# Optimization experiments

Measured on AMD Instinct MI355X. Metric: run time of the kernel, lower is better.

## Reference

```python
import jax, jax.numpy as jnp
import numpy as np

NUM_HEADS = 16
D_MODEL = 1024
D_K = D_MODEL // NUM_HEADS
MAX_SEQ_LEN = 4096
ROPE_BASE = 10000.0
BATCH = 2
SEQ_LEN = 2048


def _rope_tables(seq_len, d_k, base=ROPE_BASE):
    # theta_i = 1 / base^(2i/d_k), i = 0..d_k/2-1
    theta = 1.0 / base ** (jnp.arange(0, d_k, 2, dtype=jnp.float32) / d_k)
    m = jnp.arange(seq_len, dtype=jnp.float32)
    m_theta = jnp.outer(m, theta)                      # [S, d_k/2]
    ang = jnp.concatenate([m_theta, m_theta], axis=-1)  # [S, d_k]
    return jnp.cos(ang), jnp.sin(ang)


def _apply_rope(x, cos, sin):
    # x: [B, H, S, d_k]; rotate-half: cat(-x2, x1)
    d2 = x.shape[-1] // 2
    x1, x2 = x[..., :d2], x[..., d2:]
    x_flip = jnp.concatenate([-x2, x1], axis=-1)
    return x * cos + x_flip * sin


def setup_inputs() -> dict:
    key = jax.random.key(0)
    kx, kq, kk, kv, ko = jax.random.split(key, 5)
    s = 1.0 / np.sqrt(D_MODEL)  # ~ nn.Linear default init scale
    x = jax.random.normal(kx, (BATCH, SEQ_LEN, D_MODEL), dtype=jnp.float32)
    W_Q = jax.random.uniform(kq, (D_MODEL, D_MODEL), jnp.float32, -s, s)
    W_K = jax.random.uniform(kk, (D_MODEL, D_MODEL), jnp.float32, -s, s)
    W_V = jax.random.uniform(kv, (D_MODEL, D_MODEL), jnp.float32, -s, s)
    W_O = jax.random.uniform(ko, (D_MODEL, D_MODEL), jnp.float32, -s, s)
    return {"x": x, "W_Q": W_Q, "W_K": W_K, "W_V": W_V, "W_O": W_O}


def reference(x, W_Q, W_K, W_V, W_O):
    B, S, _ = x.shape
    # Linear with weight [out, in]: y = x @ W.T
    def proj(W):
        y = jnp.einsum('bsd,ed->bse', x, W)
        return y.reshape(B, S, NUM_HEADS, D_K).transpose(0, 2, 1, 3)  # [B,H,S,dk]
    Q, K, V = proj(W_Q), proj(W_K), proj(W_V)
    cos, sin = _rope_tables(S, D_K)
    Q = _apply_rope(Q, cos, sin)
    K = _apply_rope(K, cos, sin)
    scores = jnp.einsum('bhsd,bhtd->bhst', Q, K) / jnp.sqrt(jnp.float32(D_K))
    causal = jnp.tril(jnp.ones((S, S), dtype=bool))
    scores = jnp.where(causal[None, None], scores, -jnp.inf)
    attn = jax.nn.softmax(scores, axis=-1)
    out = jnp.einsum('bhst,bhtd->bhsd', attn, V)
    out = out.transpose(0, 2, 1, 3).reshape(B, S, D_MODEL)
    return jnp.einsum('bsd,ed->bse', out, W_O)
```

## Files before the change

### kernel.cpp

```cpp
#include <hip/hip_runtime.h>
#include <hip/hip_bf16.h>

#define BATCH 2
#define SEQ 2048
#define DM 1024
#define NH 16
#define DKH 64

typedef __attribute__((ext_vector_type(8))) __bf16 bf16x8;
typedef __attribute__((ext_vector_type(4))) float f32x4;
typedef __attribute__((ext_vector_type(2))) float f32x2;
typedef __attribute__((ext_vector_type(8))) unsigned short ushort8;

__device__ __forceinline__ void gload16(const void* g, void* l) {
  __builtin_amdgcn_global_load_lds(
      (const __attribute__((address_space(1))) void*)g,
      (__attribute__((address_space(3))) void*)l, 16, 0, 0);
}

__global__ void prep(const float* __restrict__ x,
                     const float* __restrict__ w0, const float* __restrict__ w1,
                     const float* __restrict__ w2, const float* __restrict__ w3,
                     __bf16* __restrict__ xb, __bf16* __restrict__ wb,
                     float* __restrict__ tab) {
  const int bid = blockIdx.x, tid = threadIdx.x;
  if (bid < 2048) {
    int i = bid * 256 + tid;
    f32x4 a = ((const f32x4*)x)[2 * i], b = ((const f32x4*)x)[2 * i + 1];
    bf16x8 o;
    o[0]=(__bf16)a[0]; o[1]=(__bf16)a[1]; o[2]=(__bf16)a[2]; o[3]=(__bf16)a[3];
    o[4]=(__bf16)b[0]; o[5]=(__bf16)b[1]; o[6]=(__bf16)b[2]; o[7]=(__bf16)b[3];
    ((bf16x8*)xb)[i] = o;
  } else if (bid < 4096) {
    int i = (bid - 2048) * 256 + tid;
    int wi = i >> 17;
    const float* src = (wi == 0) ? w0 : (wi == 1) ? w1 : (wi == 2) ? w2 : w3;
    int li = i & 131071;
    f32x4 a = ((const f32x4*)src)[2 * li], b = ((const f32x4*)src)[2 * li + 1];
    bf16x8 o;
    o[0]=(__bf16)a[0]; o[1]=(__bf16)a[1]; o[2]=(__bf16)a[2]; o[3]=(__bf16)a[3];
    o[4]=(__bf16)b[0]; o[5]=(__bf16)b[1]; o[6]=(__bf16)b[2]; o[7]=(__bf16)b[3];
    ((bf16x8*)wb)[i] = o;
  } else {
    int idx = (bid - 4096) * 256 + tid;
    int s = idx >> 5, ii = idx & 31;
    float theta = exp2f((float)ii * -0.41524101186092029f);
    float sn, c;
    sincosf((float)s * theta, &sn, &c);
    tab[2 * idx] = c;
    tab[2 * idx + 1] = sn;
  }
}

#define QSCALE 0.1803368801111137f

template<int EPI, int BN>
__launch_bounds__(256, 3)
__global__ void gemm_bt(const __bf16* __restrict__ A, const __bf16* __restrict__ B,
                        void* __restrict__ Cout, int M, int N, int K,
                        const float* __restrict__ tab) {
  __shared__ __bf16 As[128 * 64];
  __shared__ __bf16 Bs[BN * 64];
  const int tid = threadIdx.x;
  const int lane = tid & 63;
  const int w = tid >> 6;
  const int wr = w >> 1, wc = w & 1;
  const int fr = lane & 15, fq = lane >> 4;
  const int lid = blockIdx.y * gridDim.x + blockIdx.x;
  const int total = gridDim.x * gridDim.y;
  const int nlid = (lid >> 3) + (lid & 7) * (total >> 3);
  const int bx = nlid & 31;
  const int by = nlid >> 5;
  const int m0 = bx * 128;
  const int n0 = by * BN;
  const int NFR = BN / 32;

  f32x4 acc[4][BN / 32] = {};
  const int NT = K >> 6;

  for (int kt = 0; kt < NT; ++kt) {
    const int k0 = kt << 6;
    __syncthreads();
    #pragma unroll
    for (int p = 0; p < 4; ++p) {
      int c = p * 256 + tid;
      int row = c >> 3, cs = (c & 7) ^ (row & 7);
      gload16(&A[(size_t)(m0 + row) * K + k0 + cs * 8], &As[(p * 256 + w * 64) * 8]);
    }
    #pragma unroll
    for (int p = 0; p < BN / 32; ++p) {
      int c = p * 256 + tid;
      int row = c >> 3, cs = (c & 7) ^ (row & 7);
      gload16(&B[(size_t)(n0 + row) * K + k0 + cs * 8], &Bs[(p * 256 + w * 64) * 8]);
    }
    __syncthreads();
    #pragma unroll
    for (int kk = 0; kk < 2; ++kk) {
      bf16x8 af[4], bfr[BN / 32];
      #pragma unroll
      for (int mf = 0; mf < 4; ++mf) {
        int row = wr * 64 + mf * 16 + fr;
        af[mf] = *(const bf16x8*)&As[row * 64 + ((kk * 32 + fq * 8) ^ ((fr & 7) << 3))];
      }
      #pragma unroll
      for (int nf = 0; nf < NFR; ++nf) {
        int row = wc * (BN / 2) + nf * 16 + fr;
        bfr[nf] = *(const bf16x8*)&Bs[row * 64 + ((kk * 32 + fq * 8) ^ ((fr & 7) << 3))];
      }
      __builtin_amdgcn_s_setprio(1);
      #pragma unroll
      for (int mf = 0; mf < 4; ++mf)
        #pragma unroll
        for (int nf = 0; nf < NFR; ++nf)
          acc[mf][nf] = __builtin_amdgcn_mfma_f32_16x16x32_bf16(af[mf], bfr[nf], acc[mf][nf], 0, 0, 0);
      __builtin_amdgcn_s_setprio(0);
    }
  }

  if (EPI == 0) {
    const int nbase = n0 + wc * 64;
    const int which = nbase >> 10;
    const int h = (nbase & 1023) >> 6;
    const int b = m0 >> 11;
    __bf16* base0 = (__bf16*)Cout + (size_t)which * (4u << 20);
    if (which < 2) {
      const float scale = (which == 0) ? QSCALE : 1.0f;
      __bf16* dst = base0 + ((size_t)(b * NH + h)) * SEQ * DKH;
      #pragma unroll
      for (int mf = 0; mf < 4; ++mf) {
        #pragma unroll
        for (int j = 0; j < 4; ++j) {
          int s = (m0 & (SEQ - 1)) + wr * 64 + mf * 16 + fq * 4 + j;
          #pragma unroll
          for (int nf = 0; nf < 2; ++nf) {
            int i = nf * 16 + fr;
            f32x2 cs = ((const f32x2*)tab)[s * 32 + i];
            float a = acc[mf][nf][j], bb = acc[mf][nf + 2][j];
            dst[(size_t)s * DKH + i]      = (__bf16)((a * cs[0] - bb * cs[1]) * scale);
            dst[(size_t)s * DKH + i + 32] = (__bf16)((bb * cs[0] + a * cs[1]) * scale);
          }
        }
      }
    } else {
      __bf16* dst = base0 + ((size_t)(b * NH + h)) * DKH * SEQ;
      #pragma unroll
      for (int mf = 0; mf < 4; ++mf) {
        #pragma unroll
        for (int nf = 0; nf < 4; ++nf) {
          int dk = nf * 16 + fr;
          #pragma unroll
          for (int j = 0; j < 4; ++j) {
            int sp = (m0 & (SEQ - 1)) + wr * 64 + (mf >> 1) * 32 + fq * 8 + (mf & 1) * 4 + j;
            dst[(size_t)dk * SEQ + sp] = (__bf16)acc[mf][nf][j];
          }
        }
      }
    }
  } else {
    #pragma unroll
    for (int mf = 0; mf < 4; ++mf)
      #pragma unroll
      for (int nf = 0; nf < NFR; ++nf)
        #pragma unroll
        for (int j = 0; j < 4; ++j) {
          int m = m0 + wr * 64 + mf * 16 + fq * 4 + j;
          int n = n0 + wc * (BN / 2) + nf * 16 + fr;
          ((float*)Cout)[(size_t)m * N + n] = acc[mf][nf][j];
        }
  }
}

__launch_bounds__(512, 4)
__global__ void attn_causal(const __bf16* __restrict__ Qg, const __bf16* __restrict__ Kg,
                            const __bf16* __restrict__ Vtg, __bf16* __restrict__ Out,
                            float* __restrict__ P0, float* __restrict__ P1,
                            float* __restrict__ L0, float* __restrict__ L1) {
  __shared__ __bf16 Ks[2][128 * 64];
  __shared__ __bf16 Vts[2][64 * 128];
  const int tid = threadIdx.x;
  const int lane = tid & 63;
  const int w = tid >> 6;
  const int fr = lane & 15, fq = lane >> 4;
  const int r = blockIdx.x;
  const int nlid = (r & 7) * 64 + (r >> 3);
  const int bh = nlid >> 4;
  const int slot = nlid & 15;
  const bool isA = slot < 8;
  const int qa = slot;
  const int qb = isA ? (15 - slot) : slot;
  const int sw  = isA ? (qa + 1) : 99;
  const int off = isA ? (8 - qa) : 0;
  const int nst = isA ? 8 : 9;
  const int b = bh >> 4, h = bh & 15;
  const __bf16* Qh = Qg + (size_t)bh * SEQ * DKH;
  const __bf16* Kh = Kg + (size_t)bh * SEQ * DKH;
  const __bf16* Vth = Vtg + (size_t)bh * DKH * SEQ;

  int qrow_lo = (isA ? qa : qb) * 128 + w * 16;

  const int ck0 = tid, ck1 = 512 + tid;
  const int kr0 = ck0 >> 3, kc0 = ((ck0 & 7) ^ (kr0 & 7)) * 8;
  const int kr1 = ck1 >> 3, kc1 = ((ck1 & 7) ^ (kr1 & 7)) * 8;
  const int vd0 = ck0 >> 4, vk0 = (((ck0 & 15) & 8) | (((ck0 & 15) ^ vd0) & 7)) * 8;
  const int vd1 = ck1 >> 4, vk1 = (((ck1 & 15) & 8) | (((ck1 & 15) ^ vd1) & 7)) * 8;

#define STAGE(buf, kvt) {                                                     \
    const int ts_ = (kvt) << 7;                                               \
    gload16(&Kh[(size_t)(ts_ + kr0) * DKH + kc0], &Ks[buf][(w * 64) * 8]);    \
    gload16(&Kh[(size_t)(ts_ + kr1) * DKH + kc1], &Ks[buf][(512 + w * 64) * 8]); \
    gload16(&Vth[(size_t)vd0 * SEQ + ts_ + vk0], &Vts[buf][(w * 64) * 8]);    \
    gload16(&Vth[(size_t)vd1 * SEQ + ts_ + vk1], &Vts[buf][(512 + w * 64) * 8]); }

  bf16x8 qf[2];
  #pragma unroll
  for (int kk = 0; kk < 2; ++kk)
    qf[kk] = *(const bf16x8*)&Qh[(size_t)(qrow_lo + fr) * DKH + kk * 32 + fq * 8];

  f32x4 Oa[4] = {};
  float lsum = 0.f;

  STAGE(0, 0);
  __syncthreads();

  for (int it = 0; it < 9; ++it) {
    const int cur = it & 1;
    if (it + 1 < nst) {
      const int nx = it + 1;
      const int kvn = (nx < sw) ? nx : nx + off;
      STAGE(cur ^ 1, kvn);
    }
    if (isA && it == sw) {
      float ls = lsum;
      ls += __shfl_xor(ls, 16);
      ls += __shfl_xor(ls, 32);
      float rl[4];
      #pragma unroll
      for (int j = 0; j < 4; ++j)
        rl[j] = 1.0f / __shfl(ls, fq * 4 + j);
      #pragma unroll
      for (int nf = 0; nf < 4; ++nf)
        #pragma unroll
        for (int j = 0; j < 4; ++j) {
          int qr = qrow_lo + fq * 4 + j;
          Out[((size_t)(b * SEQ) + qr) * DM + h * DKH + nf * 16 + fr] =
              (__bf16)(Oa[nf][j] * rl[j]);
        }
      #pragma unroll
      for (int nf = 0; nf < 4; ++nf) Oa[nf] = (f32x4){0.f, 0.f, 0.f, 0.f};
      lsum = 0.f;
      qrow_lo = qb * 128 + w * 16;
      #pragma unroll
      for (int kk = 0; kk < 2; ++kk)
        qf[kk] = *(const bf16x8*)&Qh[(size_t)(qrow_lo + fr) * DKH + kk * 32 + fq * 8];
    }
    if (it < nst) {
      const int kvt = (it < sw) ? it : it + off;
      #pragma unroll
      for (int sub = 0; sub < 2; ++sub) {
        const int ts = (kvt << 7) + (sub << 6);
        if (ts > qrow_lo + 15) continue;
        f32x4 sacc[4] = {};
        __builtin_amdgcn_s_setprio(1);
        #pragma unroll
        for (int kk = 0; kk < 2; ++kk) {
          #pragma unroll
          for (int nf = 0; nf < 4; ++nf) {
            int krow = (sub << 6) + nf * 16 + fr;
            bf16x8 kf = *(const bf16x8*)&Ks[cur][krow * 64 + ((kk * 32 + fq * 8) ^ ((fr & 7) << 3))];
            sacc[nf] = __builtin_amdgcn_mfma_f32_16x16x32_bf16(kf, qf[kk], sacc[nf], 0, 0, 0);
          }
        }
        __builtin_amdgcn_s_setprio(0);
        const bool need_mask = (ts + 63 > qrow_lo);
        if (need_mask) {
          const int qr = qrow_lo + fr;
          #pragma unroll
          for (int nf = 0; nf < 4; ++nf) {
            #pragma unroll
            for (int j = 0; j < 4; ++j) {
              float v = sacc[nf][j];
              int tc = ts + nf * 16 + fq * 4 + j;
              if (tc > qr) v = -INFINITY;
              float pv = exp2f(v);
              lsum += pv;
              sacc[nf][j] = pv;
            }
          }
        } else {
          #pragma unroll
          for (int nf = 0; nf < 4; ++nf) {
            #pragma unroll
            for (int j = 0; j < 4; ++j) {
              float pv = exp2f(sacc[nf][j]);
              lsum += pv;
              sacc[nf][j] = pv;
            }
          }
        }
        bf16x8 pa[2];
        #pragma unroll
        for (int kk = 0; kk < 2; ++kk)
          #pragma unroll
          for (int e = 0; e < 8; ++e)
            pa[kk][e] = (__bf16)sacc[2 * kk + (e >> 2)][e & 3];
        __builtin_amdgcn_s_setprio(1);
        #pragma unroll
        for (int kk = 0; kk < 2; ++kk) {
          #pragma unroll
          for (int nf = 0; nf < 4; ++nf) {
            int d = nf * 16 + fr;
            bf16x8 vf = *(const bf16x8*)&Vts[cur][d * 128 + (sub << 6) +
                         (((kk * 4 + fq) ^ (fr & 7)) << 3)];
            Oa[nf] = __builtin_amdgcn_mfma_f32_16x16x32_bf16(pa[kk], vf, Oa[nf], 0, 0, 0);
          }
        }
        __builtin_amdgcn_s_setprio(0);
      }
    }
    __syncthreads();
  }
#undef STAGE
  float* P = isA ? P1 : P0;
  float* L = isA ? L1 : L0;
  const int rbase = ((bh << 3) + (qb - 8)) << 7;
  float ls = lsum;
  ls += __shfl_xor(ls, 16);
  ls += __shfl_xor(ls, 32);
  if (lane < 16) L[rbase + w * 16 + lane] = ls;
  #pragma unroll
  for (int nf = 0; nf < 4; ++nf)
    #pragma unroll
    for (int j = 0; j < 4; ++j)
      P[(size_t)(rbase + w * 16 + fq * 4 + j) * 64 + nf * 16 + fr] = Oa[nf][j];
}

__global__ void combine(const float* __restrict__ P0, const float* __restrict__ P1,
                        const float* __restrict__ L0, const float* __restrict__ L1,
                        __bf16* __restrict__ Ab) {
  int t = blockIdx.x * blockDim.x + threadIdx.x;
  int rowid = t >> 3, d0 = (t & 7) * 8;
  int bh = rowid >> 10, rem = rowid & 1023;
  int tq = rem >> 7, r = rem & 127;
  float rl = 1.0f / (L0[rowid] + L1[rowid]);
  const float* p0 = P0 + (size_t)rowid * 64 + d0;
  const float* p1 = P1 + (size_t)rowid * 64 + d0;
  f32x4 a0 = *(const f32x4*)p0, a1 = *(const f32x4*)(p0 + 4);
  f32x4 b0 = *(const f32x4*)p1, b1 = *(const f32x4*)(p1 + 4);
  bf16x8 o;
  #pragma unroll
  for (int e = 0; e < 4; ++e) {
    o[e]     = (__bf16)((a0[e] + b0[e]) * rl);
    o[e + 4] = (__bf16)((a1[e] + b1[e]) * rl);
  }
  int s = (tq + 8) * 128 + r;
  int b = bh >> 4, h = bh & 15;
  *(bf16x8*)&Ab[((size_t)b * SEQ + s) * DM + h * DKH + d0] = o;
}

extern "C" void kernel_launch(void* const* d_in, const int* in_sizes, int n_in,
                              void* d_out, int out_size, void* d_ws, size_t ws_size,
                              hipStream_t stream) {
  const float* x  = (const float*)d_in[0];
  const float* Wq = (const float*)d_in[1];
  const float* Wk = (const float*)d_in[2];
  const float* Wv = (const float*)d_in[3];
  const float* Wo = (const float*)d_in[4];

  char* ws = (char*)d_ws;
  __bf16* xb  = (__bf16*)(ws);
  __bf16* wqb = (__bf16*)(ws + ( 8u << 20));
  __bf16* wob = (__bf16*)(ws + (14u << 20));
  __bf16* Qb  = (__bf16*)(ws + (16u << 20));
  __bf16* Kb  = (__bf16*)(ws + (24u << 20));
  __bf16* Vtb = (__bf16*)(ws + (32u << 20));
  __bf16* Ab  = (__bf16*)(ws + (40u << 20));
  float*  tab = (float*)(ws + (48u << 20));
  float*  L0  = (float*)(ws + (49u << 20));
  float*  L1  = (float*)(ws + (49u << 20) + (1u << 18));
  float* P0 = (float*)d_out;
  float* P1 = P0 + (32768 * 64);

  prep<<<dim3(4352), dim3(256), 0, stream>>>(x, Wq, Wk, Wv, Wo, xb, wqb, tab);

  gemm_bt<0, 128><<<dim3(32, 24), dim3(256), 0, stream>>>(xb, wqb, Qb, BATCH * SEQ, 3 * DM, DM, tab);

  attn_causal<<<dim3(512), dim3(512), 0, stream>>>(Qb, Kb, Vtb, Ab, P0, P1, L0, L1);

  combine<<<dim3(1024), dim3(256), 0, stream>>>(P0, P1, L0, L1, Ab);

  gemm_bt<1, 64><<<dim3(32, 16), dim3(256), 0, stream>>>(Ab, wob, d_out, BATCH * SEQ, DM, DM, nullptr);
}
```

Baseline: 96.44 us.

## Fuse split-KV combine into attention via atomic flags; compute row sums with MFMA

```diff
diff --git a/kernel.cpp b/kernel.cpp
--- a/kernel.cpp
+++ b/kernel.cpp
@@ -22,7 +22,7 @@
                      const float* __restrict__ w0, const float* __restrict__ w1,
                      const float* __restrict__ w2, const float* __restrict__ w3,
                      __bf16* __restrict__ xb, __bf16* __restrict__ wb,
-                     float* __restrict__ tab) {
+                     float* __restrict__ tab, int* __restrict__ flags) {
   const int bid = blockIdx.x, tid = threadIdx.x;
   if (bid < 2048) {
     int i = bid * 256 + tid;
@@ -41,7 +41,7 @@
     o[0]=(__bf16)a[0]; o[1]=(__bf16)a[1]; o[2]=(__bf16)a[2]; o[3]=(__bf16)a[3];
     o[4]=(__bf16)b[0]; o[5]=(__bf16)b[1]; o[6]=(__bf16)b[2]; o[7]=(__bf16)b[3];
     ((bf16x8*)wb)[i] = o;
-  } else {
+  } else if (bid < 4352) {
     int idx = (bid - 4096) * 256 + tid;
     int s = idx >> 5, ii = idx & 31;
     float theta = exp2f((float)ii * -0.41524101186092029f);
@@ -49,6 +49,8 @@
     sincosf((float)s * theta, &sn, &c);
     tab[2 * idx] = c;
     tab[2 * idx + 1] = sn;
+  } else {
+    flags[tid] = 0;
   }
 }
 
@@ -174,9 +176,11 @@
 __global__ void attn_causal(const __bf16* __restrict__ Qg, const __bf16* __restrict__ Kg,
                             const __bf16* __restrict__ Vtg, __bf16* __restrict__ Out,
                             float* __restrict__ P0, float* __restrict__ P1,
-                            float* __restrict__ L0, float* __restrict__ L1) {
+                            float* __restrict__ L0, float* __restrict__ L1,
+                            int* __restrict__ flags) {
   __shared__ __bf16 Ks[2][128 * 64];
   __shared__ __bf16 Vts[2][64 * 128];
+  __shared__ int oldf;
   const int tid = threadIdx.x;
   const int lane = tid & 63;
   const int w = tid >> 6;
@@ -216,8 +220,12 @@
   for (int kk = 0; kk < 2; ++kk)
     qf[kk] = *(const bf16x8*)&Qh[(size_t)(qrow_lo + fr) * DKH + kk * 32 + fq * 8];
 
+  bf16x8 vones;
+  #pragma unroll
+  for (int e = 0; e < 8; ++e) vones[e] = (fr == 0) ? (__bf16)1.0f : (__bf16)0.0f;
+
   f32x4 Oa[4] = {};
-  float lsum = 0.f;
+  f32x4 Oa5 = {};
 
   STAGE(0, 0);
   __syncthreads();
@@ -230,13 +238,10 @@
       STAGE(cur ^ 1, kvn);
     }
     if (isA && it == sw) {
-      float ls = lsum;
-      ls += __shfl_xor(ls, 16);
-      ls += __shfl_xor(ls, 32);
       float rl[4];
       #pragma unroll
       for (int j = 0; j < 4; ++j)
-        rl[j] = 1.0f / __shfl(ls, fq * 4 + j);
+        rl[j] = 1.0f / __shfl(Oa5[j], fq << 4);
       #pragma unroll
       for (int nf = 0; nf < 4; ++nf)
         #pragma unroll
@@ -247,7 +252,7 @@
         }
       #pragma unroll
       for (int nf = 0; nf < 4; ++nf) Oa[nf] = (f32x4){0.f, 0.f, 0.f, 0.f};
-      lsum = 0.f;
+      Oa5 = (f32x4){0.f, 0.f, 0.f, 0.f};
       qrow_lo = qb * 128 + w * 16;
       #pragma unroll
       for (int kk = 0; kk < 2; ++kk)
@@ -281,20 +286,15 @@
               float v = sacc[nf][j];
               int tc = ts + nf * 16 + fq * 4 + j;
               if (tc > qr) v = -INFINITY;
-              float pv = exp2f(v);
-              lsum += pv;
-              sacc[nf][j] = pv;
+              sacc[nf][j] = exp2f(v);
             }
           }
         } else {
           #pragma unroll
           for (int nf = 0; nf < 4; ++nf) {
             #pragma unroll
-            for (int j = 0; j < 4; ++j) {
-              float pv = exp2f(sacc[nf][j]);
-              lsum += pv;
-              sacc[nf][j] = pv;
-            }
+            for (int j = 0; j < 4; ++j)
+              sacc[nf][j] = exp2f(sacc[nf][j]);
           }
         }
         bf16x8 pa[2];
@@ -313,6 +313,7 @@
                          (((kk * 4 + fq) ^ (fr & 7)) << 3)];
             Oa[nf] = __builtin_amdgcn_mfma_f32_16x16x32_bf16(pa[kk], vf, Oa[nf], 0, 0, 0);
           }
+          Oa5 = __builtin_amdgcn_mfma_f32_16x16x32_bf16(pa[kk], vones, Oa5, 0, 0, 0);
         }
         __builtin_amdgcn_s_setprio(0);
       }
@@ -322,39 +323,40 @@
 #undef STAGE
   float* P = isA ? P1 : P0;
   float* L = isA ? L1 : L0;
-  const int rbase = ((bh << 3) + (qb - 8)) << 7;
-  float ls = lsum;
-  ls += __shfl_xor(ls, 16);
-  ls += __shfl_xor(ls, 32);
-  if (lane < 16) L[rbase + w * 16 + lane] = ls;
+  const int tidx = (bh << 3) + (qb - 8);
+  const int rbase = tidx << 7;
+  if (fr == 0) {
+    #pragma unroll
+    for (int j = 0; j < 4; ++j)
+      L[rbase + w * 16 + fq * 4 + j] = Oa5[j];
+  }
   #pragma unroll
   for (int nf = 0; nf < 4; ++nf)
     #pragma unroll
     for (int j = 0; j < 4; ++j)
       P[(size_t)(rbase + w * 16 + fq * 4 + j) * 64 + nf * 16 + fr] = Oa[nf][j];
-}
-
-__global__ void combine(const float* __restrict__ P0, const float* __restrict__ P1,
-                        const float* __restrict__ L0, const float* __restrict__ L1,
-                        __bf16* __restrict__ Ab) {
-  int t = blockIdx.x * blockDim.x + threadIdx.x;
-  int rowid = t >> 3, d0 = (t & 7) * 8;
-  int bh = rowid >> 10, rem = rowid & 1023;
-  int tq = rem >> 7, r = rem & 127;
-  float rl = 1.0f / (L0[rowid] + L1[rowid]);
-  const float* p0 = P0 + (size_t)rowid * 64 + d0;
-  const float* p1 = P1 + (size_t)rowid * 64 + d0;
-  f32x4 a0 = *(const f32x4*)p0, a1 = *(const f32x4*)(p0 + 4);
-  f32x4 b0 = *(const f32x4*)p1, b1 = *(const f32x4*)(p1 + 4);
-  bf16x8 o;
-  #pragma unroll
-  for (int e = 0; e < 4; ++e) {
-    o[e]     = (__bf16)((a0[e] + b0[e]) * rl);
-    o[e + 4] = (__bf16)((a1[e] + b1[e]) * rl);
-  }
-  int s = (tq + 8) * 128 + r;
-  int b = bh >> 4, h = bh & 15;
-  *(bf16x8*)&Ab[((size_t)b * SEQ + s) * DM + h * DKH + d0] = o;
+
+  __threadfence();
+  if (tid == 0) oldf = atomicAdd(&flags[tidx], 1);
+  __syncthreads();
+  if (oldf == 1) {
+    __threadfence();
+    int row = tid >> 2, seg = tid & 3;
+    int rid = rbase + row;
+    float rl2 = 1.0f / (L0[rid] + L1[rid]);
+    const float* p0 = P0 + (size_t)rid * 64 + seg * 16;
+    const float* p1 = P1 + (size_t)rid * 64 + seg * 16;
+    bf16x8 o0, o1;
+    #pragma unroll
+    for (int e = 0; e < 8; ++e) {
+      o0[e] = (__bf16)((p0[e] + p1[e]) * rl2);
+      o1[e] = (__bf16)((p0[e + 8] + p1[e + 8]) * rl2);
+    }
+    int s = 1024 + ((qb - 8) << 7) + row;
+    __bf16* dst = Out + ((size_t)b * SEQ + s) * DM + h * DKH + seg * 16;
+    *(bf16x8*)dst = o0;
+    *(bf16x8*)(dst + 8) = o1;
+  }
 }
 
 extern "C" void kernel_launch(void* const* d_in, const int* in_sizes, int n_in,
@@ -377,16 +379,15 @@
   float*  tab = (float*)(ws + (48u << 20));
   float*  L0  = (float*)(ws + (49u << 20));
   float*  L1  = (float*)(ws + (49u << 20) + (1u << 18));
+  int*  flags = (int*)(ws + (49u << 20) + (1u << 19));
   float* P0 = (float*)d_out;
   float* P1 = P0 + (32768 * 64);
 
-  prep<<<dim3(4352), dim3(256), 0, stream>>>(x, Wq, Wk, Wv, Wo, xb, wqb, tab);
+  prep<<<dim3(4353), dim3(256), 0, stream>>>(x, Wq, Wk, Wv, Wo, xb, wqb, tab, flags);
 
   gemm_bt<0, 128><<<dim3(32, 24), dim3(256), 0, stream>>>(xb, wqb, Qb, BATCH * SEQ, 3 * DM, DM, tab);
 
-  attn_causal<<<dim3(512), dim3(512), 0, stream>>>(Qb, Kb, Vtb, Ab, P0, P1, L0, L1);
-
-  combine<<<dim3(1024), dim3(256), 0, stream>>>(P0, P1, L0, L1, Ab);
+  attn_causal<<<dim3(512), dim3(512), 0, stream>>>(Qb, Kb, Vtb, Ab, P0, P1, L0, L1, flags);
 
   gemm_bt<1, 64><<<dim3(32, 16), dim3(256), 0, stream>>>(Ab, wob, d_out, BATCH * SEQ, DM, DM, nullptr);
 }
```

New measurement: 261.8 us. +171.4%, slower.
